# Kernel tuning notes

Hardware: AMD Instinct MI355X
Metric: run time of the kernel (lower is better)

The kernel has to match this reference:

```python
import jax, jax.numpy as jnp
import numpy as np

B, H, W, C, G = 4, 56, 56, 256, 16
K = 9  # 3x3 deformable kernel
GC = C // G


def _ln(x, g, b, eps=1e-5):
    mu = jnp.mean(x, axis=-1, keepdims=True)
    var = jnp.mean(jnp.square(x - mu), axis=-1, keepdims=True)
    return (x - mu) * jax.lax.rsqrt(var + eps) * g + b


def _gelu(x):
    return jax.nn.gelu(x, approximate=False)  # torch nn.GELU default = exact erf


def _dcnv3_core(x, offset, mask):
    # x: [B,H,W,C]; offset: [B,H,W,G*K*2] (x,y per point); mask: [B,H,W,G,K] softmaxed over K
    xg = x.reshape(B, H * W, G, GC)
    off = offset.reshape(B, H, W, G, K, 2)
    dy, dx = jnp.meshgrid(jnp.arange(-1.0, 2.0), jnp.arange(-1.0, 2.0), indexing="ij")
    dx = dx.reshape(K).astype(x.dtype)
    dy = dy.reshape(K).astype(x.dtype)
    gx = jnp.arange(W, dtype=x.dtype)[None, None, :, None, None]
    gy = jnp.arange(H, dtype=x.dtype)[None, :, None, None, None]
    # sampling locations in unpadded pixel coords (zeros outside image == F.pad + zero grid_sample)
    px = gx + dx + off[..., 0]  # [B,H,W,G,K]
    py = gy + dy + off[..., 1]

    def flat(p):  # [B,H,W,G,K] -> [B, H*W*K, G]
        return p.transpose(0, 1, 2, 4, 3).reshape(B, H * W * K, G)

    pxf, pyf = flat(px), flat(py)
    x0 = jnp.floor(pxf)
    y0 = jnp.floor(pyf)
    acc = jnp.zeros((B, H * W * K, G, GC), x.dtype)
    for cx, cy in ((x0, y0), (x0 + 1, y0), (x0, y0 + 1), (x0 + 1, y0 + 1)):
        wgt = (1 - jnp.abs(pxf - cx)) * (1 - jnp.abs(pyf - cy))
        valid = ((cx >= 0) & (cx < W) & (cy >= 0) & (cy < H)).astype(x.dtype)
        idx = (jnp.clip(cy, 0, H - 1).astype(jnp.int32) * W
               + jnp.clip(cx, 0, W - 1).astype(jnp.int32))[..., None]  # [B,HWK,G,1]
        v = jnp.take_along_axis(xg, idx, axis=1)  # [B,HWK,G,GC]
        acc = acc + (wgt * valid)[..., None] * v
    mf = flat(mask)[..., None]  # [B,HWK,G,1]
    out = (acc * mf).reshape(B, H * W, K, G, GC).sum(axis=2)
    return out.reshape(B, H, W, C)


def _dcn(x, w_in, b_in, w_dw, b_dw, ln_dw_g, ln_dw_b, w_off, b_off,
         w_mask, b_mask, w_out, b_out):
    xp = x @ w_in + b_in  # input projection (value branch)
    x1 = jax.lax.conv_general_dilated(
        x, w_dw, window_strides=(1, 1), padding="SAME",
        dimension_numbers=("NHWC", "HWIO", "NHWC"), feature_group_count=C) + b_dw
    x1 = _gelu(_ln(x1, ln_dw_g, ln_dw_b))  # dw_conv -> LN -> GELU
    offset = x1 @ w_off + b_off  # [B,H,W,G*K*2]
    mask = jax.nn.softmax((x1 @ w_mask + b_mask).reshape(B, H, W, G, K), axis=-1)
    y = _dcnv3_core(xp, offset, mask)
    return y @ w_out + b_out


def _block(x, w_in, b_in, w_dw, b_dw, ln_dw_g, ln_dw_b, w_off, b_off,
           w_mask, b_mask, w_out, b_out, ln1_g, ln1_b,
           w_fc1, b_fc1, w_fc2, b_fc2, ln2_g, ln2_b, gamma1, gamma2):
    # post_norm=True: x = x + gamma1*LN1(dcn(x)); x = x + gamma2*LN2(mlp(x))
    y = _dcn(x, w_in, b_in, w_dw, b_dw, ln_dw_g, ln_dw_b, w_off, b_off,
             w_mask, b_mask, w_out, b_out)
    x = x + gamma1 * _ln(y, ln1_g, ln1_b)
    m = _gelu(x @ w_fc1 + b_fc1) @ w_fc2 + b_fc2  # MLP (dropout = identity)
    x = x + gamma2 * _ln(m, ln2_g, ln2_b)
    return x


def setup_inputs() -> dict:
    key = jax.random.key(0)
    ks = jax.random.split(key, 9)
    f = jnp.float32

    def rn(k, shape, s=0.02):
        return jax.random.normal(k, shape, dtype=f) * s

    return {
        "x": jax.random.normal(ks[0], (B, H, W, C), dtype=f),
        "w_in": rn(ks[1], (C, C)), "b_in": jnp.zeros((C,), f),
        "w_dw": rn(ks[2], (3, 3, 1, C), 0.1), "b_dw": jnp.zeros((C,), f),
        "ln_dw_g": jnp.ones((C,), f), "ln_dw_b": jnp.zeros((C,), f),
        "w_off": rn(ks[3], (C, G * K * 2)), "b_off": jnp.zeros((G * K * 2,), f),
        "w_mask": rn(ks[4], (C, G * K)), "b_mask": jnp.zeros((G * K,), f),
        "w_out": rn(ks[5], (C, C)), "b_out": jnp.zeros((C,), f),
        "ln1_g": jnp.ones((C,), f), "ln1_b": jnp.zeros((C,), f),
        "w_fc1": rn(ks[6], (C, C)), "b_fc1": jnp.zeros((C,), f),
        "w_fc2": rn(ks[7], (C, C)), "b_fc2": jnp.zeros((C,), f),
        "ln2_g": jnp.ones((C,), f), "ln2_b": jnp.zeros((C,), f),
        "gamma1": jnp.ones((C,), f), "gamma2": jnp.ones((C,), f),
    }


def reference(x, w_in, b_in, w_dw, b_dw, ln_dw_g, ln_dw_b, w_off, b_off,
              w_mask, b_mask, w_out, b_out, ln1_g, ln1_b,
              w_fc1, b_fc1, w_fc2, b_fc2, ln2_g, ln2_b, gamma1, gamma2):
    return _block(x, w_in, b_in, w_dw, b_dw, ln_dw_g, ln_dw_b, w_off, b_off,
                  w_mask, b_mask, w_out, b_out, ln1_g, ln1_b,
                  w_fc1, b_fc1, w_fc2, b_fc2, ln2_g, ln2_b, gamma1, gamma2)
```

## Files before the change

### kernel.cpp

```cpp
#include <hip/hip_runtime.h>
#include <math.h>

typedef unsigned short u16;
typedef unsigned int u32;
typedef __attribute__((ext_vector_type(8))) short short8;
typedef __attribute__((ext_vector_type(4))) float f32x4;

#define NB 4
#define NH 56
#define NW 56
#define HW2 (NH*NW)
#define NPIX (NB*HW2)

__device__ __forceinline__ u16 f2b(float f) {
  union { float f; u32 u; } a; a.f = f;
  return (u16)((a.u + 0x7FFFu + ((a.u >> 16) & 1u)) >> 16);
}
__device__ __forceinline__ float b2f(u16 v) {
  union { u32 u; float f; } a; a.u = ((u32)v) << 16; return a.f;
}
__device__ __forceinline__ float gelu_exact(float v) {
  return 0.5f * v * (1.0f + erff(v * 0.70710678118654752f));
}
__device__ __forceinline__ int xcd_swz(int bid, int nwg) {
  const int q = nwg >> 3, r = nwg & 7, x = bid & 7, j = bid >> 3;
  return (x < r ? x * (q + 1) : r * (q + 1) + (x - r) * q) + j;
}
__device__ __forceinline__ u32 swz(int r, int b) {
  return (u32)(r * 512 + ((b ^ (r & 7)) << 4));
}

__global__ __launch_bounds__(256) void prep_kernel(
    const float* __restrict__ w_in, const float* __restrict__ w_out,
    const float* __restrict__ w_fc1, const float* __restrict__ w_fc2,
    const float* __restrict__ w_off, const float* __restrict__ w_mask,
    const float* __restrict__ b_off, const float* __restrict__ b_mask,
    u16* __restrict__ wT, float* __restrict__ bias_cat)
{
  const int blk = blockIdx.x, t = threadIdx.x;
  if (blk < 1456) {
    const float* src; int n, N;
    if      (blk < 256)  { src = w_in;   n = blk;        N = 256; }
    else if (blk < 512)  { src = w_out;  n = blk - 256;  N = 256; }
    else if (blk < 768)  { src = w_fc1;  n = blk - 512;  N = 256; }
    else if (blk < 1024) { src = w_fc2;  n = blk - 768;  N = 256; }
    else if (blk < 1312) { src = w_off;  n = blk - 1024; N = 288; }
    else                 { src = w_mask; n = blk - 1312; N = 144; }
    wT[blk * 256 + t] = f2b(src[t * N + n]);
  } else {
    for (int j = t; j < 432; j += 256)
      bias_cat[j] = (j < 288) ? b_off[j] : b_mask[j - 288];
  }
}

__global__ __launch_bounds__(512) void p2_kernel(
    const float* __restrict__ xf, const u16* __restrict__ wT,
    const float* __restrict__ b_in, u16* __restrict__ xp_bf,
    const float* __restrict__ wdw, const float* __restrict__ bdw,
    const float* __restrict__ lng, const float* __restrict__ lnb,
    u16* __restrict__ x1)
{
  __shared__ u16 As[64 * 256];
  const int t = threadIdx.x;
  if (blockIdx.x < 196) {
    const int m0 = blockIdx.x * 64;
    {
      const int r = t >> 3;
      const float4* src = (const float4*)(xf + (size_t)(m0 + r) * 256);
      #pragma unroll
      for (int i = 0; i < 8; ++i) {
        const int f4 = (t & 7) + i * 8;
        float4 v = src[f4];
        uint2 pk;
        pk.x = (u32)f2b(v.x) | ((u32)f2b(v.y) << 16);
        pk.y = (u32)f2b(v.z) | ((u32)f2b(v.w) << 16);
        *(uint2*)((char*)As + swz(r, f4 >> 1) + (f4 & 1) * 8) = pk;
      }
    }
    __syncthreads();
    const int l = t & 63, w = t >> 6;
    const int wm = w >> 2, wn = w & 3;
    const int lr = l & 15, lk = l >> 4;
    const int ra0 = wm * 32 + lr, ra1 = wm * 32 + 16 + lr;
    f32x4 acc[2][4] = {};
    const u16* Bbase = wT + (size_t)(wn * 64 + lr) * 256 + lk * 8;
    #pragma unroll
    for (int ks = 0; ks < 8; ++ks) {
      short8 a0 = *(const short8*)((char*)As + swz(ra0, ks * 4 + lk));
      short8 a1 = *(const short8*)((char*)As + swz(ra1, ks * 4 + lk));
      #pragma unroll
      for (int ni = 0; ni < 4; ++ni) {
        short8 b = *(const short8*)(Bbase + ni * 16 * 256 + ks * 32);
        acc[0][ni] = __builtin_amdgcn_mfma_f32_16x16x32_bf16(a0, b, acc[0][ni], 0, 0, 0);
        acc[1][ni] = __builtin_amdgcn_mfma_f32_16x16x32_bf16(a1, b, acc[1][ni], 0, 0, 0);
      }
    }
    const int colb = wn * 64 + lr;
    #pragma unroll
    for (int mi = 0; mi < 2; ++mi)
      #pragma unroll
      for (int r4 = 0; r4 < 4; ++r4) {
        const int row = m0 + wm * 32 + mi * 16 + lk * 4 + r4;
        #pragma unroll
        for (int ni = 0; ni < 4; ++ni)
          xp_bf[(size_t)row * 256 + colb + ni * 16] = f2b(acc[mi][ni][r4] + b_in[colb + ni * 16]);
      }
  } else {
    const int pb = xcd_swz((int)blockIdx.x - 196, 1568);
    const int p = pb * 8 + (t >> 6);
    const int lane = t & 63, c0 = lane * 4;
    const int bb = p / HW2, hw = p - bb * HW2;
    const int h = hw / NW, w = hw - h * NW;
    float4 bd = *(const float4*)(bdw + c0);
    float a0 = bd.x, a1 = bd.y, a2 = bd.z, a3 = bd.w;
    #pragma unroll
    for (int kh = 0; kh < 3; ++kh) {
      const int hh = h + kh - 1;
      if ((unsigned)hh >= NH) continue;
      #pragma unroll
      for (int kw = 0; kw < 3; ++kw) {
        const int ww = w + kw - 1;
        if ((unsigned)ww >= NW) continue;
        float4 v = *(const float4*)(xf + (size_t)(bb * HW2 + hh * NW + ww) * 256 + c0);
        float4 wv = *(const float4*)(wdw + (kh * 3 + kw) * 256 + c0);
        a0 += v.x * wv.x; a1 += v.y * wv.y;
        a2 += v.z * wv.z; a3 += v.w * wv.w;
      }
    }
    float s1 = a0 + a1 + a2 + a3;
    float s2 = a0 * a0 + a1 * a1 + a2 * a2 + a3 * a3;
    #pragma unroll
    for (int d = 1; d < 64; d <<= 1) { s1 += __shfl_xor(s1, d); s2 += __shfl_xor(s2, d); }
    const float mu = s1 * (1.0f / 256.0f);
    const float var = s2 * (1.0f / 256.0f) - mu * mu;
    const float rs = rsqrtf(var + 1e-5f);
    float4 lg4 = *(const float4*)(lng + c0);
    float4 lb4 = *(const float4*)(lnb + c0);
    ushort4 o;
    o.x = f2b(gelu_exact((a0 - mu) * rs * lg4.x + lb4.x));
    o.y = f2b(gelu_exact((a1 - mu) * rs * lg4.y + lb4.y));
    o.z = f2b(gelu_exact((a2 - mu) * rs * lg4.z + lb4.z));
    o.w = f2b(gelu_exact((a3 - mu) * rs * lg4.w + lb4.w));
    *(ushort4*)(x1 + (size_t)p * 256 + c0) = o;
  }
}

__global__ __launch_bounds__(256) void gemm_om(
    const u16* __restrict__ A, const u16* __restrict__ Bt,
    const float* __restrict__ bias, u16* __restrict__ Cb, int Ntot)
{
  __shared__ u16 lds[32768];
  char* As = (char*)lds;
  char* Bs = (char*)(lds + 16384);
  const int nN = (Ntot + 63) >> 6;
  const int sb = xcd_swz(blockIdx.x, gridDim.x);
  const int m0 = (sb / nN) * 64;
  const int n0 = (sb % nN) * 64;
  const int t  = threadIdx.x;
  {
    const int r = t >> 2, c0 = t & 3;
    const u16* Ag = A + (size_t)(m0 + r) * 256;
    const int nrow = n0 + r;
    const u16* Bg = Bt + (size_t)nrow * 256;
    const bool bok = nrow < Ntot;
    #pragma unroll
    for (int i = 0; i < 8; ++i) {
      const int b = c0 + i * 4;
      uint4 av = *(const uint4*)(Ag + b * 8);
      *(uint4*)(As + swz(r, b)) = av;
      uint4 bv = make_uint4(0u, 0u, 0u, 0u);
      if (bok) bv = *(const uint4*)(Bg + b * 8);
      *(uint4*)(Bs + swz(r, b)) = bv;
    }
  }
  __syncthreads();
  const int l = t & 63, w = t >> 6;
  const int wm = (w >> 1) << 5, wn = (w & 1) << 5;
  const int lr = l & 15, lk = l >> 4;
  const int ra0 = wm + lr, ra1 = wm + 16 + lr;
  const int rb0 = wn + lr, rb1 = wn + 16 + lr;
  f32x4 acc00 = {}, acc01 = {}, acc10 = {}, acc11 = {};
  #pragma unroll
  for (int ks = 0; ks < 8; ++ks) {
    const int bb = ks * 4 + lk;
    short8 a0 = *(const short8*)(As + swz(ra0, bb));
    short8 a1 = *(const short8*)(As + swz(ra1, bb));
    short8 b0 = *(const short8*)(Bs + swz(rb0, bb));
    short8 b1 = *(const short8*)(Bs + swz(rb1, bb));
    acc00 = __builtin_amdgcn_mfma_f32_16x16x32_bf16(a0, b0, acc00, 0, 0, 0);
    acc01 = __builtin_amdgcn_mfma_f32_16x16x32_bf16(a0, b1, acc01, 0, 0, 0);
    acc10 = __builtin_amdgcn_mfma_f32_16x16x32_bf16(a1, b0, acc10, 0, 0, 0);
    acc11 = __builtin_amdgcn_mfma_f32_16x16x32_bf16(a1, b1, acc11, 0, 0, 0);
  }
  const f32x4 accs[2][2] = {{acc00, acc01}, {acc10, acc11}};
  #pragma unroll
  for (int mi = 0; mi < 2; ++mi)
    #pragma unroll
    for (int ni = 0; ni < 2; ++ni) {
      const int col = n0 + wn + ni * 16 + lr;
      if (col < Ntot) {
        const float bv = bias[col];
        #pragma unroll
        for (int r4 = 0; r4 < 4; ++r4) {
          const int row = m0 + wm + mi * 16 + lk * 4 + r4;
          Cb[(size_t)row * Ntot + col] = f2b(accs[mi][ni][r4] + bv);
        }
      }
    }
}

__global__ __launch_bounds__(256) void dcnv3_kernel(
    const u16* __restrict__ xp, const u16* __restrict__ omb,
    u16* __restrict__ y)
{
  __shared__ u16 lom[8 * 432];
  const int sb = xcd_swz(blockIdx.x, NPIX / 8);
  const int p0 = sb * 8;
  for (int i = threadIdx.x; i < 432; i += 256) {
    const int row = i / 54, u = i - row * 54;
    *(uint4*)(lom + row * 432 + u * 8) =
        *(const uint4*)(omb + (size_t)(p0 + row) * 432 + u * 8);
  }
  __syncthreads();
  const int tid = threadIdx.x;
  const int lp = tid >> 5, gh = tid & 31;
  const int g = gh >> 1, hf = gh & 1;
  const int p = p0 + lp;
  const int bb = p / HW2, hw = p - bb * HW2;
  const int h = hw / NW, w = hw - h * NW;
  const u16* off = lom + lp * 432 + g * 18;
  const u16* mk  = lom + lp * 432 + 288 + g * 9;
  float lg[9];
  float mx = -1e30f;
  #pragma unroll
  for (int k = 0; k < 9; ++k) { lg[k] = b2f(mk[k]); mx = fmaxf(mx, lg[k]); }
  float se = 0.0f;
  #pragma unroll
  for (int k = 0; k < 9; ++k) { lg[k] = __expf(lg[k] - mx); se += lg[k]; }
  const float inv = 1.0f / se;

  float a[8] = {0.f,0.f,0.f,0.f,0.f,0.f,0.f,0.f};
  const u16* base = xp + ((size_t)bb * HW2) * 256 + g * 16 + hf * 8;
  #pragma unroll
  for (int k = 0; k < 9; ++k) {
    const float px = (float)(w + (k % 3) - 1) + b2f(off[2 * k]);
    const float py = (float)(h + (k / 3) - 1) + b2f(off[2 * k + 1]);
    const float fx = floorf(px), fy = floorf(py);
    const int ix = (int)fx, iy = (int)fy;
    const float ax = px - fx, ay = py - fy;
    const float mwt = lg[k] * inv;
    const float w00 = (1.0f - ax) * (1.0f - ay) * mwt;
    const float w10 = ax * (1.0f - ay) * mwt;
    const float w01 = (1.0f - ax) * ay * mwt;
    const float w11 = ax * ay * mwt;
    auto corner = [&](int cx, int cy, float wt) {
      if (cx < 0 || cx >= NW || cy < 0 || cy >= NH) return;
      uint4 v = *(const uint4*)(base + (size_t)(cy * NW + cx) * 256);
      const u32 wv[4] = {v.x, v.y, v.z, v.w};
      #pragma unroll
      for (int j = 0; j < 4; ++j) {
        union { u32 u; float f; } lo, hi;
        lo.u = wv[j] << 16; hi.u = wv[j] & 0xffff0000u;
        a[2 * j]     += wt * lo.f;
        a[2 * j + 1] += wt * hi.f;
      }
    };
    corner(ix,     iy,     w00);
    corner(ix + 1, iy,     w10);
    corner(ix,     iy + 1, w01);
    corner(ix + 1, iy + 1, w11);
  }
  u16 tmp[8];
  #pragma unroll
  for (int j = 0; j < 8; ++j) tmp[j] = f2b(a[j]);
  *(uint4*)(y + ((size_t)p * 256 + g * 16 + hf * 8)) = *(const uint4*)(tmp);
}

__global__ __launch_bounds__(512) void mega3_kernel(
    const u16* __restrict__ ybf, const u16* __restrict__ wT,
    const float* __restrict__ x, const float* __restrict__ b_out,
    const float* __restrict__ gamma1, const float* __restrict__ ln1g,
    const float* __restrict__ ln1b, const float* __restrict__ b_fc1,
    const float* __restrict__ b_fc2, const float* __restrict__ gamma2,
    const float* __restrict__ ln2g, const float* __restrict__ ln2b,
    float* __restrict__ out)
{
  __shared__ u16 As[64 * 256];
  __shared__ float redS[64][4], redQ[64][4];
  const int t = threadIdx.x;
  const int m0 = blockIdx.x * 64;
  const int l = t & 63, w = t >> 6;
  const int wm = w >> 2, wn = w & 3;
  const int lr = l & 15, lk = l >> 4;
  const int ra0 = wm * 32 + lr, ra1 = wm * 32 + 16 + lr;
  const int colb = wn * 64 + lr;

  {
    const int r = t >> 3, j0 = (t & 7) * 4;
    const uint4* src = (const uint4*)(ybf + (size_t)(m0 + r) * 256);
    #pragma unroll
    for (int i = 0; i < 4; ++i)
      *(uint4*)((char*)As + swz(r, j0 + i)) = src[j0 + i];
  }
  __syncthreads();

  f32x4 acc[2][4];
  auto do_gemm = [&](const u16* Bt) {
    #pragma unroll
    for (int mi = 0; mi < 2; ++mi)
      #pragma unroll
      for (int ni = 0; ni < 4; ++ni) acc[mi][ni] = (f32x4){0.f,0.f,0.f,0.f};
    const u16* Bbase = Bt + (size_t)(wn * 64 + lr) * 256 + lk * 8;
    #pragma unroll
    for (int ks = 0; ks < 8; ++ks) {
      short8 a0 = *(const short8*)((char*)As + swz(ra0, ks * 4 + lk));
      short8 a1 = *(const short8*)((char*)As + swz(ra1, ks * 4 + lk));
      #pragma unroll
      for (int ni = 0; ni < 4; ++ni) {
        short8 b = *(const short8*)(Bbase + ni * 16 * 256 + ks * 32);
        acc[0][ni] = __builtin_amdgcn_mfma_f32_16x16x32_bf16(a0, b, acc[0][ni], 0, 0, 0);
        acc[1][ni] = __builtin_amdgcn_mfma_f32_16x16x32_bf16(a1, b, acc[1][ni], 0, 0, 0);
      }
    }
  };
  auto lds_write_b16 = [&](int row, int col, u16 v) {
    *(u16*)((char*)As + row * 512 + (((col >> 3) ^ (row & 7)) << 4) + (col & 7) * 2) = v;
  };
  auto ln_reduce = [&](const float bv[4], float s1[2][4], float s2[2][4]) {
    #pragma unroll
    for (int mi = 0; mi < 2; ++mi)
      #pragma unroll
      for (int r4 = 0; r4 < 4; ++r4) {
        float s = 0.f, q = 0.f;
        #pragma unroll
        for (int ni = 0; ni < 4; ++ni) {
          const float v = acc[mi][ni][r4] + bv[ni];
          s += v; q += v * v;
        }
        s1[mi][r4] = s; s2[mi][r4] = q;
      }
    #pragma unroll
    for (int d = 1; d < 16; d <<= 1)
      #pragma unroll
      for (int mi = 0; mi < 2; ++mi)
        #pragma unroll
        for (int r4 = 0; r4 < 4; ++r4) {
          s1[mi][r4] += __shfl_xor(s1[mi][r4], d);
          s2[mi][r4] += __shfl_xor(s2[mi][r4], d);
        }
    if (lr == 0) {
      #pragma unroll
      for (int mi = 0; mi < 2; ++mi)
        #pragma unroll
        for (int r4 = 0; r4 < 4; ++r4) {
          const int rl = wm * 32 + mi * 16 + lk * 4 + r4;
          redS[rl][wn] = s1[mi][r4];
          redQ[rl][wn] = s2[mi][r4];
        }
    }
    __syncthreads();
  };

  do_gemm(wT + 256 * 256);
  float bv1[4], s1[2][4], s2[2][4];
  #pragma unroll
  for (int ni = 0; ni < 4; ++ni) bv1[ni] = b_out[colb + ni * 16];
  ln_reduce(bv1, s1, s2);

  float x2r[2][4][4];
  {
    float gmv[4], lgv[4], lbv[4];
    #pragma unroll
    for (int ni = 0; ni < 4; ++ni) {
      gmv[ni] = gamma1[colb + ni * 16];
      lgv[ni] = ln1g[colb + ni * 16];
      lbv[ni] = ln1b[colb + ni * 16];
    }
    #pragma unroll
    for (int mi = 0; mi < 2; ++mi)
      #pragma unroll
      for (int r4 = 0; r4 < 4; ++r4) {
        const int rl = wm * 32 + mi * 16 + lk * 4 + r4;
        const float S = redS[rl][0] + redS[rl][1] + redS[rl][2] + redS[rl][3];
        const float Q = redQ[rl][0] + redQ[rl][1] + redQ[rl][2] + redQ[rl][3];
        const float mu = S * (1.0f / 256.0f);
        const float var = Q * (1.0f / 256.0f) - mu * mu;
        const float rs = rsqrtf(var + 1e-5f);
        const int row = m0 + rl;
        #pragma unroll
        for (int ni = 0; ni < 4; ++ni) {
          const float v = acc[mi][ni][r4] + bv1[ni];
          const float o = x[(size_t)row * 256 + colb + ni * 16]
                        + gmv[ni] * ((v - mu) * rs * lgv[ni] + lbv[ni]);
          x2r[mi][r4][ni] = o;
          lds_write_b16(rl, colb + ni * 16, f2b(o));
        }
      }
  }
  __syncthreads();

  do_gemm(wT + 512 * 256);
  float m1v[2][4][4];
  #pragma unroll
  for (int mi = 0; mi < 2; ++mi)
    #pragma unroll
    for (int r4 = 0; r4 < 4; ++r4)
      #pragma unroll
      for (int ni = 0; ni < 4; ++ni)
        m1v[mi][r4][ni] = gelu_exact(acc[mi][ni][r4] + b_fc1[colb + ni * 16]);
  __syncthreads();
  #pragma unroll
  for (int mi = 0; mi < 2; ++mi)
    #pragma unroll
    for (int r4 = 0; r4 < 4; ++r4) {
      const int rl = wm * 32 + mi * 16 + lk * 4 + r4;
      #pragma unroll
      for (int ni = 0; ni < 4; ++ni)
        lds_write_b16(rl, colb + ni * 16, f2b(m1v[mi][r4][ni]));
    }
  __syncthreads();

  do_gemm(wT + 768 * 256);
  float bv3[4];
  #pragma unroll
  for (int ni = 0; ni < 4; ++ni) bv3[ni] = b_fc2[colb + ni * 16];
  ln_reduce(bv3, s1, s2);
  {
    float gmv[4], lgv[4], lbv[4];
    #pragma unroll
    for (int ni = 0; ni < 4; ++ni) {
      gmv[ni] = gamma2[colb + ni * 16];
      lgv[ni] = ln2g[colb + ni * 16];
      lbv[ni] = ln2b[colb + ni * 16];
    }
    #pragma unroll
    for (int mi = 0; mi < 2; ++mi)
      #pragma unroll
      for (int r4 = 0; r4 < 4; ++r4) {
        const int rl = wm * 32 + mi * 16 + lk * 4 + r4;
        const float S = redS[rl][0] + redS[rl][1] + redS[rl][2] + redS[rl][3];
        const float Q = redQ[rl][0] + redQ[rl][1] + redQ[rl][2] + redQ[rl][3];
        const float mu = S * (1.0f / 256.0f);
        const float var = Q * (1.0f / 256.0f) - mu * mu;
        const float rs = rsqrtf(var + 1e-5f);
        const int row = m0 + rl;
        #pragma unroll
        for (int ni = 0; ni < 4; ++ni) {
          const float v = acc[mi][ni][r4] + bv3[ni];
          out[(size_t)row * 256 + colb + ni * 16] =
              x2r[mi][r4][ni] + gmv[ni] * ((v - mu) * rs * lgv[ni] + lbv[ni]);
        }
      }
  }
}

static constexpr size_t OFF_WT  = 0;
static constexpr size_t OFF_BC  = 745472;
static constexpr size_t OFF_XP  = 747520;
static constexpr size_t OFF_X1  = 7170048;
static constexpr size_t OFF_OMB = 13592576;
static constexpr size_t OFF_Y   = 24430592;

extern "C" void kernel_launch(void* const* d_in, const int* in_sizes, int n_in,
                              void* d_out, int out_size, void* d_ws, size_t ws_size,
                              hipStream_t stream)
{
  const float* x      = (const float*)d_in[0];
  const float* w_in   = (const float*)d_in[1];
  const float* b_in   = (const float*)d_in[2];
  const float* w_dw   = (const float*)d_in[3];
  const float* b_dw   = (const float*)d_in[4];
  const float* ln_dw_g= (const float*)d_in[5];
  const float* ln_dw_b= (const float*)d_in[6];
  const float* w_off  = (const float*)d_in[7];
  const float* b_off  = (const float*)d_in[8];
  const float* w_mask = (const float*)d_in[9];
  const float* b_mask = (const float*)d_in[10];
  const float* w_out  = (const float*)d_in[11];
  const float* b_out  = (const float*)d_in[12];
  const float* ln1_g  = (const float*)d_in[13];
  const float* ln1_b  = (const float*)d_in[14];
  const float* w_fc1  = (const float*)d_in[15];
  const float* b_fc1  = (const float*)d_in[16];
  const float* w_fc2  = (const float*)d_in[17];
  const float* b_fc2  = (const float*)d_in[18];
  const float* ln2_g  = (const float*)d_in[19];
  const float* ln2_b  = (const float*)d_in[20];
  const float* gamma1 = (const float*)d_in[21];
  const float* gamma2 = (const float*)d_in[22];
  float* out = (float*)d_out;

  char* ws = (char*)d_ws;
  u16*   wT    = (u16*)  (ws + OFF_WT);
  float* bcat  = (float*)(ws + OFF_BC);
  u16*   xp_bf = (u16*)  (ws + OFF_XP);
  u16*   x1    = (u16*)  (ws + OFF_X1);
  u16*   omb   = (u16*)  (ws + OFF_OMB);
  u16*   ybf   = (u16*)  (ws + OFF_Y);

  prep_kernel<<<dim3(1457), 256, 0, stream>>>(
      w_in, w_out, w_fc1, w_fc2, w_off, w_mask, b_off, b_mask, wT, bcat);
  p2_kernel<<<dim3(196 + 1568), 512, 0, stream>>>(
      x, wT, b_in, xp_bf, w_dw, b_dw, ln_dw_g, ln_dw_b, x1);
  gemm_om<<<dim3(196 * 7), 256, 0, stream>>>(x1, wT + 1024 * 256, bcat, omb, 432);
  dcnv3_kernel<<<dim3(NPIX / 8), 256, 0, stream>>>(xp_bf, omb, ybf);
  mega3_kernel<<<dim3(196), 512, 0, stream>>>(
      ybf, wT, x, b_out, gamma1, ln1_g, ln1_b, b_fc1, b_fc2,
      gamma2, ln2_g, ln2_b, out);
}
```

Measured before the change: 101.1 us.

## Regroup launches: fuse weight prep with depthwise conv, input GEMM with offset GEMM

Reorganizes the first three launches into two. The weight transpose/convert blocks now share a launch with the depthwise conv+LN+GELU blocks, and the input projection GEMM (now 64x64 tiles, 256 threads, converting fp32 input on the fly) shares a launch with the offset/mask GEMM. This cuts one kernel launch and balances work across the grid. The cost is that the input projection now runs after the depthwise stage rather than overlapping with it, and it uses smaller tiles with more redundant A loads.

```diff
diff --git a/kernel.cpp b/kernel.cpp
--- a/kernel.cpp
+++ b/kernel.cpp
@@ -30,12 +30,15 @@
   return (u32)(r * 512 + ((b ^ (r & 7)) << 4));
 }
 
-__global__ __launch_bounds__(256) void prep_kernel(
+__global__ __launch_bounds__(256) void k1_kernel(
     const float* __restrict__ w_in, const float* __restrict__ w_out,
     const float* __restrict__ w_fc1, const float* __restrict__ w_fc2,
     const float* __restrict__ w_off, const float* __restrict__ w_mask,
     const float* __restrict__ b_off, const float* __restrict__ b_mask,
-    u16* __restrict__ wT, float* __restrict__ bias_cat)
+    u16* __restrict__ wT, float* __restrict__ bias_cat,
+    const float* __restrict__ xf, const float* __restrict__ wdw,
+    const float* __restrict__ bdw, const float* __restrict__ lng,
+    const float* __restrict__ lnb, u16* __restrict__ x1)
 {
   const int blk = blockIdx.x, t = threadIdx.x;
   if (blk < 1456) {
@@ -47,67 +50,12 @@
     else if (blk < 1312) { src = w_off;  n = blk - 1024; N = 288; }
     else                 { src = w_mask; n = blk - 1312; N = 144; }
     wT[blk * 256 + t] = f2b(src[t * N + n]);
-  } else {
+  } else if (blk == 1456) {
     for (int j = t; j < 432; j += 256)
       bias_cat[j] = (j < 288) ? b_off[j] : b_mask[j - 288];
-  }
-}
-
-__global__ __launch_bounds__(512) void p2_kernel(
-    const float* __restrict__ xf, const u16* __restrict__ wT,
-    const float* __restrict__ b_in, u16* __restrict__ xp_bf,
-    const float* __restrict__ wdw, const float* __restrict__ bdw,
-    const float* __restrict__ lng, const float* __restrict__ lnb,
-    u16* __restrict__ x1)
-{
-  __shared__ u16 As[64 * 256];
-  const int t = threadIdx.x;
-  if (blockIdx.x < 196) {
-    const int m0 = blockIdx.x * 64;
-    {
-      const int r = t >> 3;
-      const float4* src = (const float4*)(xf + (size_t)(m0 + r) * 256);
-      #pragma unroll
-      for (int i = 0; i < 8; ++i) {
-        const int f4 = (t & 7) + i * 8;
-        float4 v = src[f4];
-        uint2 pk;
-        pk.x = (u32)f2b(v.x) | ((u32)f2b(v.y) << 16);
-        pk.y = (u32)f2b(v.z) | ((u32)f2b(v.w) << 16);
-        *(uint2*)((char*)As + swz(r, f4 >> 1) + (f4 & 1) * 8) = pk;
-      }
-    }
-    __syncthreads();
-    const int l = t & 63, w = t >> 6;
-    const int wm = w >> 2, wn = w & 3;
-    const int lr = l & 15, lk = l >> 4;
-    const int ra0 = wm * 32 + lr, ra1 = wm * 32 + 16 + lr;
-    f32x4 acc[2][4] = {};
-    const u16* Bbase = wT + (size_t)(wn * 64 + lr) * 256 + lk * 8;
-    #pragma unroll
-    for (int ks = 0; ks < 8; ++ks) {
-      short8 a0 = *(const short8*)((char*)As + swz(ra0, ks * 4 + lk));
-      short8 a1 = *(const short8*)((char*)As + swz(ra1, ks * 4 + lk));
-      #pragma unroll
-      for (int ni = 0; ni < 4; ++ni) {
-        short8 b = *(const short8*)(Bbase + ni * 16 * 256 + ks * 32);
-        acc[0][ni] = __builtin_amdgcn_mfma_f32_16x16x32_bf16(a0, b, acc[0][ni], 0, 0, 0);
-        acc[1][ni] = __builtin_amdgcn_mfma_f32_16x16x32_bf16(a1, b, acc[1][ni], 0, 0, 0);
-      }
-    }
-    const int colb = wn * 64 + lr;
-    #pragma unroll
-    for (int mi = 0; mi < 2; ++mi)
-      #pragma unroll
-      for (int r4 = 0; r4 < 4; ++r4) {
-        const int row = m0 + wm * 32 + mi * 16 + lk * 4 + r4;
-        #pragma unroll
-        for (int ni = 0; ni < 4; ++ni)
-          xp_bf[(size_t)row * 256 + colb + ni * 16] = f2b(acc[mi][ni][r4] + b_in[colb + ni * 16]);
-      }
   } else {
-    const int pb = xcd_swz((int)blockIdx.x - 196, 1568);
-    const int p = pb * 8 + (t >> 6);
+    const int pb = xcd_swz(blk - 1457, 3136);
+    const int p = pb * 4 + (t >> 6);
     const int lane = t & 63, c0 = lane * 4;
     const int bb = p / HW2, hw = p - bb * HW2;
     const int h = hw / NW, w = hw - h * NW;
@@ -145,29 +93,41 @@
   }
 }
 
-__global__ __launch_bounds__(256) void gemm_om(
-    const u16* __restrict__ A, const u16* __restrict__ Bt,
-    const float* __restrict__ bias, u16* __restrict__ Cb, int Ntot)
-{
-  __shared__ u16 lds[32768];
-  char* As = (char*)lds;
-  char* Bs = (char*)(lds + 16384);
-  const int nN = (Ntot + 63) >> 6;
-  const int sb = xcd_swz(blockIdx.x, gridDim.x);
-  const int m0 = (sb / nN) * 64;
-  const int n0 = (sb % nN) * 64;
-  const int t  = threadIdx.x;
+template<int AF32>
+__device__ __forceinline__ void gemm64_body(
+    const void* __restrict__ Asrc, const u16* __restrict__ Brows,
+    const float* __restrict__ bias, u16* __restrict__ Cout,
+    int Ntot, int m0, int n0, char* As, char* Bs, int t)
+{
+  if (AF32) {
+    const int r = t >> 2;
+    const float4* src = (const float4*)((const float*)Asrc + (size_t)(m0 + r) * 256);
+    #pragma unroll
+    for (int i = 0; i < 16; ++i) {
+      const int f4 = (t & 3) + i * 4;
+      float4 v = src[f4];
+      uint2 pk;
+      pk.x = (u32)f2b(v.x) | ((u32)f2b(v.y) << 16);
+      pk.y = (u32)f2b(v.z) | ((u32)f2b(v.w) << 16);
+      *(uint2*)(As + swz(r, f4 >> 1) + (f4 & 1) * 8) = pk;
+    }
+  } else {
+    const int r = t >> 2, c0 = t & 3;
+    const u16* Ag = (const u16*)Asrc + (size_t)(m0 + r) * 256;
+    #pragma unroll
+    for (int i = 0; i < 8; ++i) {
+      const int b = c0 + i * 4;
+      *(uint4*)(As + swz(r, b)) = *(const uint4*)(Ag + b * 8);
+    }
+  }
   {
     const int r = t >> 2, c0 = t & 3;
-    const u16* Ag = A + (size_t)(m0 + r) * 256;
     const int nrow = n0 + r;
-    const u16* Bg = Bt + (size_t)nrow * 256;
+    const u16* Bg = Brows + (size_t)nrow * 256;
     const bool bok = nrow < Ntot;
     #pragma unroll
     for (int i = 0; i < 8; ++i) {
       const int b = c0 + i * 4;
-      uint4 av = *(const uint4*)(Ag + b * 8);
-      *(uint4*)(As + swz(r, b)) = av;
       uint4 bv = make_uint4(0u, 0u, 0u, 0u);
       if (bok) bv = *(const uint4*)(Bg + b * 8);
       *(uint4*)(Bs + swz(r, b)) = bv;
@@ -203,10 +163,31 @@
         #pragma unroll
         for (int r4 = 0; r4 < 4; ++r4) {
           const int row = m0 + wm + mi * 16 + lk * 4 + r4;
-          Cb[(size_t)row * Ntot + col] = f2b(accs[mi][ni][r4] + bv);
-        }
-      }
-    }
+          Cout[(size_t)row * Ntot + col] = f2b(accs[mi][ni][r4] + bv);
+        }
+      }
+    }
+}
+
+__global__ __launch_bounds__(256) void k2_kernel(
+    const float* __restrict__ xf, const u16* __restrict__ x1,
+    const u16* __restrict__ wT, const float* __restrict__ b_in,
+    const float* __restrict__ bcat, u16* __restrict__ xp_bf,
+    u16* __restrict__ omb)
+{
+  __shared__ u16 lds[32768];
+  char* As = (char*)lds;
+  char* Bs = (char*)(lds + 16384);
+  const int t = threadIdx.x;
+  if (blockIdx.x < 784) {
+    const int sb = xcd_swz(blockIdx.x, 784);
+    const int m0 = (sb >> 2) * 64, n0 = (sb & 3) * 64;
+    gemm64_body<1>(xf, wT, b_in, xp_bf, 256, m0, n0, As, Bs, t);
+  } else {
+    const int sb = xcd_swz((int)blockIdx.x - 784, 1372);
+    const int m0 = (sb / 7) * 64, n0 = (sb % 7) * 64;
+    gemm64_body<0>(x1, wT + 1024 * 256, bcat, omb, 432, m0, n0, As, Bs, t);
+  }
 }
 
 __global__ __launch_bounds__(256) void dcnv3_kernel(
@@ -498,11 +479,11 @@
   u16*   omb   = (u16*)  (ws + OFF_OMB);
   u16*   ybf   = (u16*)  (ws + OFF_Y);
 
-  prep_kernel<<<dim3(1457), 256, 0, stream>>>(
-      w_in, w_out, w_fc1, w_fc2, w_off, w_mask, b_off, b_mask, wT, bcat);
-  p2_kernel<<<dim3(196 + 1568), 512, 0, stream>>>(
-      x, wT, b_in, xp_bf, w_dw, b_dw, ln_dw_g, ln_dw_b, x1);
-  gemm_om<<<dim3(196 * 7), 256, 0, stream>>>(x1, wT + 1024 * 256, bcat, omb, 432);
+  k1_kernel<<<dim3(1457 + 3136), 256, 0, stream>>>(
+      w_in, w_out, w_fc1, w_fc2, w_off, w_mask, b_off, b_mask, wT, bcat,
+      x, w_dw, b_dw, ln_dw_g, ln_dw_b, x1);
+  k2_kernel<<<dim3(784 + 1372), 256, 0, stream>>>(
+      x, x1, wT, b_in, bcat, xp_bf, omb);
   dcnv3_kernel<<<dim3(NPIX / 8), 256, 0, stream>>>(xp_bf, omb, ybf);
   mega3_kernel<<<dim3(196), 512, 0, stream>>>(
       ybf, wT, x, b_out, gamma1, ln1_g, ln1_b, b_fc1, b_fc2,
```

Measured after the change: 93.46 us. -7.6%, faster.
